# Performance work log

Hardware: AMD Instinct MI355X
Metric: run time of the kernel (lower is better)

Reference implementation:

```python
import jax, jax.numpy as jnp
import numpy as np

N = 16
FS = 48000
NFFT = FS * 8            # irfft length hard-coded in the module
F = NFFT // 2 + 1        # 192001 frequency sample points
DELAYS = [809, 877, 937, 1049, 1151, 1249, 1373, 1499,
          1617, 1753, 1879, 2003, 2131, 2269, 2393, 2521]
GAIN_PER_SAMPLE = 0.9998


def setup_inputs() -> dict:
    key = jax.random.key(0)
    k1, k2, k3 = jax.random.split(key, 3)
    # frequency sample points on the upper half of the unit circle (rfft bins)
    omega = jnp.linspace(0.0, np.pi, F).astype(jnp.float32)
    x_real = jnp.cos(omega)
    x_imag = jnp.sin(omega)
    B = jax.random.normal(k1, (1, N, 1), dtype=jnp.float32) / N
    C = jax.random.normal(k2, (1, 1, N), dtype=jnp.float32) / N
    X = jax.random.normal(k3, (N, N), dtype=jnp.float32)  # raw Linear weight (pre-parametrization)
    return {"x_real": x_real, "x_imag": x_imag, "B": B, "C": C, "X": X}


def _delays_m():
    # torch does (m - mean)/std then forward undoes it: m = m_norm*std + mean
    m = jnp.asarray(DELAYS, dtype=jnp.float32)
    mStd = jnp.std(m, ddof=1)   # torch.std is unbiased
    mAvr = jnp.mean(m)
    m_norm = (m - mAvr) / mStd
    return m_norm * mStd + mAvr


def reference(x_real, x_imag, B, C, X):
    x = (x_real + 1j * x_imag).astype(jnp.complex64)          # [F]
    # Skew -> matrix_exp parametrization: A = expm(triu(X,1) - triu(X,1)^T), orthogonal
    Au = jnp.triu(X, 1)
    A = jax.scipy.linalg.expm(Au - Au.T)                       # [N, N]
    m = _delays_m()                                            # [N] float delays
    gamma = jnp.asarray(GAIN_PER_SAMPLE, jnp.float32) ** m     # diag of Gamma, [N]
    AG = (A * gamma[None, :]).astype(jnp.complex64)            # A @ diag(gamma), [N, N]
    # D = diag_embed(x[:,None] ** m) ; build (D - A Gamma) fused
    Dd = x[:, None] ** m[None, :]                              # [F, N] complex
    M = Dd[:, :, None] * jnp.eye(N, dtype=jnp.complex64) - AG[None, :, :]  # [F, N, N]
    Bc = B.astype(jnp.complex64)                               # [1, N, 1], broadcasts over F
    Hch = jnp.linalg.solve(M, Bc)                              # [F, N, 1]  == inv(M) @ B
    H = Hch[:, :, 0] * C.astype(jnp.complex64).reshape(1, N)   # [F, N]
    Hs = jnp.sum(H, axis=-1)                                   # [F]
    mask = jnp.where(x == 0, 0.0, 1.0).astype(jnp.complex64)   # H_mask zeroing x==0 bins
    h = jnp.fft.irfft(Hs * mask, n=NFFT)                       # [NFFT] real
    h = h / jnp.max(jnp.abs(h))
    return H, h
```

## Files before the change

kernel.cpp:

```cpp
#include <hip/hip_runtime.h>
#include <math.h>

#define NN 16
#define FF 192001
#define NFFTN 384000
#define N1F 1024
#define N2F 375
#define TWO_PI 6.283185307179586476925286766559

__constant__ float c_delays[16] = {809.f, 877.f, 937.f, 1049.f, 1151.f, 1249.f, 1373.f, 1499.f,
                                   1617.f, 1753.f, 1879.f, 2003.f, 2131.f, 2269.f, 2393.f, 2521.f};
__constant__ int c_idelays[16] = {809, 877, 937, 1049, 1151, 1249, 1373, 1499,
                                  1617, 1753, 1879, 2003, 2131, 2269, 2393, 2521};

__device__ __forceinline__ float fastrcp(float x) {
#if __has_builtin(__builtin_amdgcn_rcpf)
  return __builtin_amdgcn_rcpf(x);
#else
  return 1.0f / x;
#endif
}

__global__ void expm_kernel(const float* __restrict__ X, float* __restrict__ AGout) {
  __shared__ double S[16][16], P[16][16], E[16][16];
  const int i = threadIdx.x >> 4, j = threadIdx.x & 15;
  double xu = (j > i) ? (double)X[i * 16 + j] : 0.0;
  double xl = (i > j) ? (double)X[j * 16 + i] : 0.0;
  double s = (xu - xl) * (1.0 / 256.0);
  S[i][j] = s;
  P[i][j] = s;
  E[i][j] = (i == j ? 1.0 : 0.0) + s;
  __syncthreads();
  for (int k = 2; k <= 24; ++k) {
    double acc = 0.0;
#pragma unroll
    for (int l = 0; l < 16; ++l) acc += P[i][l] * S[l][j];
    acc /= (double)k;
    __syncthreads();
    P[i][j] = acc;
    E[i][j] += acc;
    __syncthreads();
  }
  for (int t = 0; t < 8; ++t) {
    double acc = 0.0;
#pragma unroll
    for (int l = 0; l < 16; ++l) acc += E[i][l] * E[l][j];
    __syncthreads();
    E[i][j] = acc;
    __syncthreads();
  }
  double g = exp((double)c_delays[j] * log(0.9998));
  AGout[i * 16 + j] = (float)(E[i][j] * g);
}

template <int K>
__device__ __forceinline__ float2 bc16(float2 v) {
  float2 o;
  o.x = __int_as_float(__builtin_amdgcn_ds_swizzle(__float_as_int(v.x), (K << 5) | 0x10));
  o.y = __int_as_float(__builtin_amdgcn_ds_swizzle(__float_as_int(v.y), (K << 5) | 0x10));
  return o;
}

template <int K>
__device__ __forceinline__ void gj_step(float2 (&reg)[17], const int r) {
  float2 pk = bc16<K>(reg[K]);
  float invd = fastrcp(pk.x * pk.x + pk.y * pk.y);
  float rcx = pk.x * invd, rcy = -pk.y * invd;
  const bool ispiv = (r == K);
  float frx = ispiv ? (1.0f - rcx) : (reg[K].x * rcx - reg[K].y * rcy);
  float fry = ispiv ? (-rcy) : (reg[K].x * rcy + reg[K].y * rcx);
#pragma unroll
  for (int c = K + 1; c < 17; ++c) {
    float2 pc = bc16<K>(reg[c]);
    reg[c].x -= frx * pc.x - fry * pc.y;
    reg[c].y -= frx * pc.y + fry * pc.x;
  }
}

template <int K>
struct GJAll {
  static __device__ __forceinline__ void run(float2 (&reg)[17], int r) {
    gj_step<K>(reg, r);
    GJAll<K + 1>::run(reg, r);
  }
};
template <>
struct GJAll<16> {
  static __device__ __forceinline__ void run(float2 (&)[17], int) {}
};

template <bool CPLX>
__global__ __launch_bounds__(256, 6) void solve_kernel(
    const float* __restrict__ Bv, const float* __restrict__ Cv,
    const float* __restrict__ AGin, float* __restrict__ Hout,
    float2* __restrict__ G) {
  __shared__ float AGp[16][17];
  __shared__ float Bs[16], Cs[16];
  const int tid = threadIdx.x;
  AGp[tid >> 4][tid & 15] = AGin[tid];
  if (tid < 16) { Bs[tid] = Bv[tid]; Cs[tid] = Cv[tid]; }
  const int r = tid & 15;
  int f = blockIdx.x * 16 + (tid >> 4);
  const bool active = (f < FF);
  if (!active) f = FF - 1;
  __syncthreads();

  int ph = (c_idelays[r] * f) % NFFTN;
  float th = (float)ph * (float)(TWO_PI / (double)NFFTN);
  float si, co;
  sincosf(th, &si, &co);

  float2 reg[17];
#pragma unroll
  for (int c = 0; c < 16; ++c) {
    float re = -AGp[r][c];
    float im = 0.0f;
    if (c == r) { re += co; im = si; }
    reg[c] = make_float2(re, im);
  }
  reg[16] = make_float2(Bs[r], 0.0f);

  GJAll<0>::run(reg, r);

  const float cc = Cs[r];
  float2 h = make_float2(reg[16].x * cc, reg[16].y * cc);
  if (active) {
    if (CPLX) {
      ((float2*)Hout)[(size_t)f * 16 + r] = h;
    } else {
      Hout[(size_t)f * 16 + r] = h.x;
    }
  }
  float sx = h.x, sy = h.y;
#pragma unroll
  for (int off = 8; off > 0; off >>= 1) {
    sx += __shfl_xor(sx, off, 16);
    sy += __shfl_xor(sy, off, 16);
  }
  if (active && r == 0) {
    if (f == 0 || f == 192000) sy = 0.0f;
    G[f] = make_float2(sx, sy);
    if (f > 0 && f < 192000) G[NFFTN - f] = make_float2(sx, -sy);
  }
}

__global__ __launch_bounds__(256) void fftA_kernel(const float2* __restrict__ G,
                                                   float2* __restrict__ Bb) {
  __shared__ float2 buf[2][1024];
  const int k2 = blockIdx.x;
  const int tid = threadIdx.x;
#pragma unroll
  for (int rr = 0; rr < 4; ++rr) {
    int k1 = tid + 256 * rr;
    buf[0][k1] = G[k2 + 375 * k1];
  }
  __syncthreads();
  int src = 0, nt = 1024, s = 1;
  for (int st = 0; st < 10; ++st) {
    int m = nt >> 1;
#pragma unroll
    for (int rr = 0; rr < 2; ++rr) {
      int jj = tid + 256 * rr;
      int p = jj >> st;
      int q = jj & (s - 1);
      float ang = (float)p * (6.28318530717958647692f / (float)nt);
      float ws_, wc_;
      sincosf(ang, &ws_, &wc_);
      float2 a = buf[src][q + s * p];
      float2 b = buf[src][q + s * (p + m)];
      float2 sum = make_float2(a.x + b.x, a.y + b.y);
      float2 d = make_float2(a.x - b.x, a.y - b.y);
      float2 wd = make_float2(d.x * wc_ - d.y * ws_, d.x * ws_ + d.y * wc_);
      buf[src ^ 1][q + s * (2 * p)] = sum;
      buf[src ^ 1][q + s * (2 * p + 1)] = wd;
    }
    __syncthreads();
    src ^= 1;
    nt >>= 1;
    s <<= 1;
  }
  const double tw0 = TWO_PI * (double)k2 / (double)NFFTN;
#pragma unroll
  for (int rr = 0; rr < 4; ++rr) {
    int t1 = tid + 256 * rr;
    float2 vz = buf[src][t1];
    float a = (float)(tw0 * (double)t1);
    float sn, cs;
    sincosf(a, &sn, &cs);
    Bb[t1 * 375 + k2] = make_float2(vz.x * cs - vz.y * sn, vz.x * sn + vz.y * cs);
  }
}

__global__ __launch_bounds__(384) void fftB_kernel(const float2* __restrict__ Bb,
                                                   float* __restrict__ hout) {
  __shared__ float2 bv[375];
  __shared__ float2 tw[375];
  __shared__ float2 Y[375];
  const int t1 = blockIdx.x;
  const int tid = threadIdx.x;
  if (tid < 375) {
    bv[tid] = Bb[t1 * 375 + tid];
    float ang = (float)(TWO_PI * (double)tid / 375.0);
    float s, c;
    sincosf(ang, &s, &c);
    tw[tid] = make_float2(c, s);
  }
  __syncthreads();
  if (tid < 375) {
    const int a = tid / 15, u = tid - 15 * a;
    float ax = 0.f, ay = 0.f;
    int i15 = 0;
#pragma unroll
    for (int b = 0; b < 15; ++b) {
      float2 x = bv[a + 25 * b];
      float2 w = tw[i15 * 25];
      ax += x.x * w.x - x.y * w.y;
      ay += x.x * w.y + x.y * w.x;
      i15 += u;
      if (i15 >= 15) i15 -= 15;
    }
    Y[tid] = make_float2(ax, ay);
  }
  __syncthreads();
  if (tid < 375) {
    const int t = tid;
    const int u = t % 15;
    float acc = 0.f;
    int idx = 0;
#pragma unroll
    for (int a = 0; a < 25; ++a) {
      float2 y = Y[a * 15 + u];
      float2 w = tw[idx];
      acc += y.x * w.x - y.y * w.y;
      idx += t;
      if (idx >= 375) idx -= 375;
    }
    hout[t1 + 1024 * t] = acc * (1.0f / (float)NFFTN);
  }
}

__global__ void max_kernel(const float* __restrict__ h, unsigned* __restrict__ mx) {
  float m = 0.0f;
  for (int i = blockIdx.x * blockDim.x + threadIdx.x; i < NFFTN;
       i += gridDim.x * blockDim.x)
    m = fmaxf(m, fabsf(h[i]));
#pragma unroll
  for (int off = 32; off > 0; off >>= 1) m = fmaxf(m, __shfl_xor(m, off, 64));
  if ((threadIdx.x & 63) == 0) atomicMax(mx, __float_as_uint(m));
}

__global__ void norm_kernel(float* __restrict__ h, const unsigned* __restrict__ mx) {
  int i = blockIdx.x * blockDim.x + threadIdx.x;
  float mv = __uint_as_float(*mx);
  if (i < NFFTN) h[i] = h[i] / mv;
}

extern "C" void kernel_launch(void* const* d_in, const int* in_sizes, int n_in,
                              void* d_out, int out_size, void* d_ws, size_t ws_size,
                              hipStream_t stream) {
  (void)in_sizes; (void)n_in; (void)ws_size;
  const float* Bv = (const float*)d_in[2];
  const float* Cv = (const float*)d_in[3];
  const float* X  = (const float*)d_in[4];
  float* out = (float*)d_out;
  char* ws = (char*)d_ws;
  float2* G    = (float2*)(ws);
  float2* Bb   = (float2*)(ws + 3072000);
  unsigned* mx = (unsigned*)(ws + 6144000);
  float*  AGw  = (float*)(ws + 6144064);

  float* htail = out + (out_size - NFFTN);

  hipMemsetAsync(mx, 0, 4, stream);
  expm_kernel<<<1, 256, 0, stream>>>(X, AGw);
  if (out_size >= 2 * FF * NN + NFFTN) {
    solve_kernel<true><<<(FF + 15) / 16, 256, 0, stream>>>(Bv, Cv, AGw, out, G);
  } else {
    solve_kernel<false><<<(FF + 15) / 16, 256, 0, stream>>>(Bv, Cv, AGw, out, G);
  }
  fftA_kernel<<<N2F, 256, 0, stream>>>(G, Bb);
  fftB_kernel<<<N1F, 384, 0, stream>>>(Bb, htail);
  max_kernel<<<256, 256, 0, stream>>>(htail, mx);
  norm_kernel<<<1500, 256, 0, stream>>>(htail, mx);
}
```

Baseline: 191.1 us.

## Process two matrix rows per lane in solve, fuse max into fftB, drop memset

The Gauss-Jordan solve now assigns two rows per lane (8 lanes per frequency instead of 16), so one pivot broadcast serves two rows. Updates use packed float2 FMAs, which may map to packed-math instructions. This halves the swizzle count per frequency and doubles the frequencies per block, at the cost of more registers (occupancy hint lowered from 6 to 4). The abs-max reduction is also fused into the fftB kernel with a block-level reduce and one atomic per block, and the mx reset moves into expm_kernel. That removes the separate max kernel and the memset launch.

```diff
diff --git a/kernel.cpp b/kernel.cpp
--- a/kernel.cpp
+++ b/kernel.cpp
@@ -13,6 +13,8 @@
 __constant__ int c_idelays[16] = {809, 877, 937, 1049, 1151, 1249, 1373, 1499,
                                   1617, 1753, 1879, 2003, 2131, 2269, 2393, 2521};
 
+typedef float v2f __attribute__((ext_vector_type(2)));
+
 __device__ __forceinline__ float fastrcp(float x) {
 #if __has_builtin(__builtin_amdgcn_rcpf)
   return __builtin_amdgcn_rcpf(x);
@@ -21,7 +23,9 @@
 #endif
 }
 
-__global__ void expm_kernel(const float* __restrict__ X, float* __restrict__ AGout) {
+__global__ void expm_kernel(const float* __restrict__ X, float* __restrict__ AGout,
+                            unsigned* __restrict__ mx) {
+  if (threadIdx.x == 0) *mx = 0u;
   __shared__ double S[16][16], P[16][16], E[16][16];
   const int i = threadIdx.x >> 4, j = threadIdx.x & 15;
   double xu = (j > i) ? (double)X[i * 16 + j] : 0.0;
@@ -53,44 +57,64 @@
   AGout[i * 16 + j] = (float)(E[i][j] * g);
 }
 
+template <int S>
+__device__ __forceinline__ v2f bc8(v2f v) {
+  v2f o;
+  o[0] = __int_as_float(__builtin_amdgcn_ds_swizzle(__float_as_int(v[0]), (S << 5) | 0x18));
+  o[1] = __int_as_float(__builtin_amdgcn_ds_swizzle(__float_as_int(v[1]), (S << 5) | 0x18));
+  return o;
+}
+
+template <int K, int C>
+struct ColLoop {
+  static __device__ __forceinline__ void run(v2f (&A)[17], v2f (&B)[17],
+                                             v2f nA0, v2f A1, v2f nB0, v2f B1) {
+    v2f pc;
+    if constexpr (K & 1) pc = bc8<(K >> 1)>(B[C]);
+    else                 pc = bc8<(K >> 1)>(A[C]);
+    v2f pcs = {pc[1], pc[0]};
+    A[C] = __builtin_elementwise_fma(nA0, pc, A[C]);
+    A[C] = __builtin_elementwise_fma(A1, pcs, A[C]);
+    B[C] = __builtin_elementwise_fma(nB0, pc, B[C]);
+    B[C] = __builtin_elementwise_fma(B1, pcs, B[C]);
+    ColLoop<K, C + 1>::run(A, B, nA0, A1, nB0, B1);
+  }
+};
 template <int K>
-__device__ __forceinline__ float2 bc16(float2 v) {
-  float2 o;
-  o.x = __int_as_float(__builtin_amdgcn_ds_swizzle(__float_as_int(v.x), (K << 5) | 0x10));
-  o.y = __int_as_float(__builtin_amdgcn_ds_swizzle(__float_as_int(v.y), (K << 5) | 0x10));
-  return o;
-}
+struct ColLoop<K, 17> {
+  static __device__ __forceinline__ void run(v2f (&)[17], v2f (&)[17], v2f, v2f, v2f, v2f) {}
+};
 
 template <int K>
-__device__ __forceinline__ void gj_step(float2 (&reg)[17], const int r) {
-  float2 pk = bc16<K>(reg[K]);
-  float invd = fastrcp(pk.x * pk.x + pk.y * pk.y);
-  float rcx = pk.x * invd, rcy = -pk.y * invd;
-  const bool ispiv = (r == K);
-  float frx = ispiv ? (1.0f - rcx) : (reg[K].x * rcx - reg[K].y * rcy);
-  float fry = ispiv ? (-rcy) : (reg[K].x * rcy + reg[K].y * rcx);
-#pragma unroll
-  for (int c = K + 1; c < 17; ++c) {
-    float2 pc = bc16<K>(reg[c]);
-    reg[c].x -= frx * pc.x - fry * pc.y;
-    reg[c].y -= frx * pc.y + fry * pc.x;
-  }
-}
-
-template <int K>
-struct GJAll {
-  static __device__ __forceinline__ void run(float2 (&reg)[17], int r) {
-    gj_step<K>(reg, r);
-    GJAll<K + 1>::run(reg, r);
+struct GJStep8 {
+  static __device__ __forceinline__ void run(v2f (&A)[17], v2f (&B)[17], int s) {
+    constexpr int S = K >> 1;
+    v2f pk;
+    if constexpr (K & 1) pk = bc8<S>(B[K]);
+    else                 pk = bc8<S>(A[K]);
+    float invd = fastrcp(pk[0] * pk[0] + pk[1] * pk[1]);
+    float rcx = pk[0] * invd, rcy = -pk[1] * invd;
+    bool ispA, ispB;
+    if constexpr (K & 1) { ispA = false; ispB = (s == S); }
+    else                 { ispA = (s == S); ispB = false; }
+    v2f mA = A[K], mB = B[K];
+    float frAx = ispA ? (1.0f - rcx) : (mA[0] * rcx - mA[1] * rcy);
+    float frAy = ispA ? (-rcy)       : (mA[0] * rcy + mA[1] * rcx);
+    float frBx = ispB ? (1.0f - rcx) : (mB[0] * rcx - mB[1] * rcy);
+    float frBy = ispB ? (-rcy)       : (mB[0] * rcy + mB[1] * rcx);
+    v2f nA0 = {-frAx, -frAx}, A1 = {frAy, -frAy};
+    v2f nB0 = {-frBx, -frBx}, B1 = {frBy, -frBy};
+    ColLoop<K, K + 1>::run(A, B, nA0, A1, nB0, B1);
+    GJStep8<K + 1>::run(A, B, s);
   }
 };
 template <>
-struct GJAll<16> {
-  static __device__ __forceinline__ void run(float2 (&)[17], int) {}
+struct GJStep8<16> {
+  static __device__ __forceinline__ void run(v2f (&)[17], v2f (&)[17], int) {}
 };
 
 template <bool CPLX>
-__global__ __launch_bounds__(256, 6) void solve_kernel(
+__global__ __launch_bounds__(256, 4) void solve_kernel(
     const float* __restrict__ Bv, const float* __restrict__ Cv,
     const float* __restrict__ AGin, float* __restrict__ Hout,
     float2* __restrict__ G) {
@@ -99,45 +123,57 @@
   const int tid = threadIdx.x;
   AGp[tid >> 4][tid & 15] = AGin[tid];
   if (tid < 16) { Bs[tid] = Bv[tid]; Cs[tid] = Cv[tid]; }
-  const int r = tid & 15;
-  int f = blockIdx.x * 16 + (tid >> 4);
+  const int s = tid & 7;
+  const int a = 2 * s, b = a + 1;
+  int f = blockIdx.x * 32 + (tid >> 3);
   const bool active = (f < FF);
   if (!active) f = FF - 1;
   __syncthreads();
 
-  int ph = (c_idelays[r] * f) % NFFTN;
-  float th = (float)ph * (float)(TWO_PI / (double)NFFTN);
-  float si, co;
-  sincosf(th, &si, &co);
-
-  float2 reg[17];
+  int pa = (c_idelays[a] * f) % NFFTN;
+  int pb = (c_idelays[b] * f) % NFFTN;
+  float tha = (float)pa * (float)(TWO_PI / (double)NFFTN);
+  float thb = (float)pb * (float)(TWO_PI / (double)NFFTN);
+  float sa, ca, sb, cb;
+  sincosf(tha, &sa, &ca);
+  sincosf(thb, &sb, &cb);
+
+  v2f A[17], B[17];
 #pragma unroll
   for (int c = 0; c < 16; ++c) {
-    float re = -AGp[r][c];
-    float im = 0.0f;
-    if (c == r) { re += co; im = si; }
-    reg[c] = make_float2(re, im);
-  }
-  reg[16] = make_float2(Bs[r], 0.0f);
-
-  GJAll<0>::run(reg, r);
-
-  const float cc = Cs[r];
-  float2 h = make_float2(reg[16].x * cc, reg[16].y * cc);
+    float reA = -AGp[a][c], imA = 0.0f;
+    float reB = -AGp[b][c], imB = 0.0f;
+    if ((c & 1) == 0) {
+      if (c == a) { reA += ca; imA = sa; }
+    } else {
+      if (c == b) { reB += cb; imB = sb; }
+    }
+    A[c] = (v2f){reA, imA};
+    B[c] = (v2f){reB, imB};
+  }
+  A[16] = (v2f){Bs[a], 0.0f};
+  B[16] = (v2f){Bs[b], 0.0f};
+
+  GJStep8<0>::run(A, B, s);
+
+  const float cca = Cs[a], ccb = Cs[b];
+  v2f hA = {A[16][0] * cca, A[16][1] * cca};
+  v2f hB = {B[16][0] * ccb, B[16][1] * ccb};
   if (active) {
     if (CPLX) {
-      ((float2*)Hout)[(size_t)f * 16 + r] = h;
+      ((float2*)Hout)[(size_t)f * 16 + a] = make_float2(hA[0], hA[1]);
+      ((float2*)Hout)[(size_t)f * 16 + b] = make_float2(hB[0], hB[1]);
     } else {
-      Hout[(size_t)f * 16 + r] = h.x;
-    }
-  }
-  float sx = h.x, sy = h.y;
-#pragma unroll
-  for (int off = 8; off > 0; off >>= 1) {
-    sx += __shfl_xor(sx, off, 16);
-    sy += __shfl_xor(sy, off, 16);
-  }
-  if (active && r == 0) {
+      *(float2*)&Hout[(size_t)f * 16 + a] = make_float2(hA[0], hB[0]);
+    }
+  }
+  float sx = hA[0] + hB[0], sy = hA[1] + hB[1];
+#pragma unroll
+  for (int off = 4; off > 0; off >>= 1) {
+    sx += __shfl_xor(sx, off, 8);
+    sy += __shfl_xor(sy, off, 8);
+  }
+  if (active && s == 0) {
     if (f == 0 || f == 192000) sy = 0.0f;
     G[f] = make_float2(sx, sy);
     if (f > 0 && f < 192000) G[NFFTN - f] = make_float2(sx, -sy);
@@ -192,10 +228,12 @@
 }
 
 __global__ __launch_bounds__(384) void fftB_kernel(const float2* __restrict__ Bb,
-                                                   float* __restrict__ hout) {
+                                                   float* __restrict__ hout,
+                                                   unsigned* __restrict__ mx) {
   __shared__ float2 bv[375];
   __shared__ float2 tw[375];
   __shared__ float2 Y[375];
+  __shared__ float wmax[6];
   const int t1 = blockIdx.x;
   const int tid = threadIdx.x;
   if (tid < 375) {
@@ -222,6 +260,7 @@
     Y[tid] = make_float2(ax, ay);
   }
   __syncthreads();
+  float m = 0.0f;
   if (tid < 375) {
     const int t = tid;
     const int u = t % 15;
@@ -235,18 +274,20 @@
       idx += t;
       if (idx >= 375) idx -= 375;
     }
-    hout[t1 + 1024 * t] = acc * (1.0f / (float)NFFTN);
-  }
-}
-
-__global__ void max_kernel(const float* __restrict__ h, unsigned* __restrict__ mx) {
-  float m = 0.0f;
-  for (int i = blockIdx.x * blockDim.x + threadIdx.x; i < NFFTN;
-       i += gridDim.x * blockDim.x)
-    m = fmaxf(m, fabsf(h[i]));
+    float hv = acc * (1.0f / (float)NFFTN);
+    hout[t1 + 1024 * t] = hv;
+    m = fabsf(hv);
+  }
 #pragma unroll
   for (int off = 32; off > 0; off >>= 1) m = fmaxf(m, __shfl_xor(m, off, 64));
-  if ((threadIdx.x & 63) == 0) atomicMax(mx, __float_as_uint(m));
+  if ((tid & 63) == 0) wmax[tid >> 6] = m;
+  __syncthreads();
+  if (tid == 0) {
+    float mm = wmax[0];
+#pragma unroll
+    for (int w = 1; w < 6; ++w) mm = fmaxf(mm, wmax[w]);
+    atomicMax(mx, __float_as_uint(mm));
+  }
 }
 
 __global__ void norm_kernel(float* __restrict__ h, const unsigned* __restrict__ mx) {
@@ -271,15 +312,13 @@
 
   float* htail = out + (out_size - NFFTN);
 
-  hipMemsetAsync(mx, 0, 4, stream);
-  expm_kernel<<<1, 256, 0, stream>>>(X, AGw);
+  expm_kernel<<<1, 256, 0, stream>>>(X, AGw, mx);
   if (out_size >= 2 * FF * NN + NFFTN) {
-    solve_kernel<true><<<(FF + 15) / 16, 256, 0, stream>>>(Bv, Cv, AGw, out, G);
+    solve_kernel<true><<<(FF + 31) / 32, 256, 0, stream>>>(Bv, Cv, AGw, out, G);
   } else {
-    solve_kernel<false><<<(FF + 15) / 16, 256, 0, stream>>>(Bv, Cv, AGw, out, G);
+    solve_kernel<false><<<(FF + 31) / 32, 256, 0, stream>>>(Bv, Cv, AGw, out, G);
   }
   fftA_kernel<<<N2F, 256, 0, stream>>>(G, Bb);
-  fftB_kernel<<<N1F, 384, 0, stream>>>(Bb, htail);
-  max_kernel<<<256, 256, 0, stream>>>(htail, mx);
+  fftB_kernel<<<N1F, 384, 0, stream>>>(Bb, htail, mx);
   norm_kernel<<<1500, 256, 0, stream>>>(htail, mx);
 }
```

After: 166.1 us. 1.15x faster.
